# Performance work log

Measured on AMD Instinct MI355X. Metric: run time of the kernel, lower is better.

The kernel has to match this reference:

```python
import jax, jax.numpy as jnp
import numpy as np

N = 200000
C = 128
VOX = 0.05
EPS = 1e-5
OFFSETS = np.array([[dz, dy, dx] for dz in (-1, 0, 1) for dy in (-1, 0, 1) for dx in (-1, 0, 1)], dtype=np.int64)


def setup_inputs() -> dict:
    key = jax.random.key(0)
    ks = jax.random.split(key, 8)
    gp = jax.random.normal(ks[0], (N, 14), jnp.float32)
    # ---- voxelization tables (int constants, computed once in numpy) ----
    pts = np.asarray(gp[:, :3], dtype=np.float64)
    vc = np.floor(pts / VOX).astype(np.int64)
    vc = vc - vc.min(axis=0)
    mx = vc.max(axis=0) + 1
    h = vc[:, 0] * mx[1] * mx[2] + vc[:, 1] * mx[2] + vc[:, 2]
    uh, inv = np.unique(h, return_inverse=True)
    M = int(uh.shape[0])
    vcoord = np.zeros((M, 3), np.int64)
    vcoord[inv] = vc  # coords identical for same hash
    nbr_idx = np.zeros((M, 27), np.int32)
    nbr_mask = np.zeros((M, 27), np.float32)
    for o in range(27):
        nc = vcoord + OFFSETS[o]
        inb = (nc >= 0).all(1) & (nc < mx).all(1)
        nh = nc[:, 0] * mx[1] * mx[2] + nc[:, 1] * mx[2] + nc[:, 2]
        pos = np.clip(np.searchsorted(uh, nh), 0, M - 1)
        found = inb & (uh[pos] == nh)
        nbr_idx[:, o] = np.where(found, pos, 0)
        nbr_mask[:, o] = found.astype(np.float32)
    s = 0.05
    return {
        'gaussian_params': gp,
        'w_enc': jax.random.normal(ks[1], (14, C), jnp.float32) * s,
        'b_enc': jnp.zeros((C,), jnp.float32),
        'ln_g': jnp.ones((C,), jnp.float32),
        'ln_b': jnp.zeros((C,), jnp.float32),
        'conv_w': jax.random.normal(ks[2], (4, 27, C, C), jnp.float32) * s,
        'bn_g': jnp.ones((4, C), jnp.float32),
        'bn_b': jnp.zeros((4, C), jnp.float32),
        'w1': jax.random.normal(ks[3], (C, C // 2), jnp.float32) * s,
        'b1': jnp.zeros((C // 2,), jnp.float32),
        'w2': jax.random.normal(ks[4], (C // 2, 14), jnp.float32) * s,
        'b2': jnp.zeros((14,), jnp.float32),
        'nbr_mask': jnp.asarray(nbr_mask),
        'inv_idx': jnp.asarray(inv.astype(np.int32)),
        'nbr_idx': jnp.asarray(nbr_idx),
        'num_voxels': M,
    }


def _bn(x, g, b):
    m = x.mean(0)
    v = x.var(0)
    return (x - m) * jax.lax.rsqrt(v + EPS) * g + b


def _subm(x, W, nbr_idx, nbr_mask):
    # submanifold 3x3x3 conv: sum over 27 offsets of masked neighbor gather @ W[o]
    out = jnp.zeros_like(x)
    for o in range(27):
        out = out + (x[nbr_idx[:, o]] * nbr_mask[:, o:o + 1]) @ W[o]
    return out


def _forward(gp, w_enc, b_enc, ln_g, ln_b, conv_w, bn_g, bn_b, w1, b1, w2, b2, nbr_mask, inv_idx, nbr_idx, num_voxels):
    # input encoder: Linear -> LayerNorm -> ReLU
    f = gp @ w_enc + b_enc
    mu = f.mean(-1, keepdims=True)
    var = f.var(-1, keepdims=True)
    f = jax.nn.relu((f - mu) * jax.lax.rsqrt(var + EPS) * ln_g + ln_b)
    # points -> voxels: segment mean (the op the torch code did with a Python loop)
    cnt = jax.ops.segment_sum(jnp.ones((gp.shape[0],), f.dtype), inv_idx, num_segments=num_voxels)
    x = jax.ops.segment_sum(f, inv_idx, num_segments=num_voxels) / cnt[:, None]
    # 2 residual sparse conv blocks (BN uses batch stats, training-mode forward)
    for blk in range(2):
        idn = x
        out = _subm(x, conv_w[2 * blk], nbr_idx, nbr_mask)
        out = jax.nn.relu(_bn(out, bn_g[2 * blk], bn_b[2 * blk]))
        out = _subm(out, conv_w[2 * blk + 1], nbr_idx, nbr_mask)
        x = jax.nn.relu(_bn(out, bn_g[2 * blk + 1], bn_b[2 * blk + 1]) + idn)
    # voxels -> points, output head, residual add
    pf = x[inv_idx]
    delta = jax.nn.relu(pf @ w1 + b1) @ w2 + b2
    return gp[:, :14] + delta


def reference(gaussian_params, w_enc, b_enc, ln_g, ln_b, conv_w, bn_g, bn_b, w1, b1, w2, b2, nbr_mask, inv_idx, nbr_idx, num_voxels):
    return _forward(gaussian_params, w_enc, b_enc, ln_g, ln_b, conv_w, bn_g, bn_b, w1, b1, w2, b2, nbr_mask, inv_idx, nbr_idx, num_voxels)
```

## Files before the change

kernel.cpp:

```cpp
#include <hip/hip_runtime.h>

typedef __bf16 bf16x8 __attribute__((ext_vector_type(8)));
typedef float f32x16 __attribute__((ext_vector_type(16)));

#define LN_EPS 1e-5f
#define AS1 __attribute__((address_space(1)))
#define AS3 __attribute__((address_space(3)))

__device__ __forceinline__ unsigned f2bf_rne(float f) {
    unsigned x = __float_as_uint(f);
    return (x + 0x7fffu + ((x >> 16) & 1u)) >> 16;
}

__device__ __forceinline__ float bf2f(unsigned short u) {
    return __uint_as_float((unsigned)u << 16);
}

__global__ void pack_w_kernel(const float* __restrict__ cw, unsigned short* __restrict__ Wp, int E) {
    int idx = blockIdx.x * 256 + threadIdx.x;
    if (idx >= E) return;
    float v = cw[idx];
    int n  = idx & 127;
    int c  = (idx >> 7) & 127;
    int oc = idx >> 14;
    Wp[oc * 16384 + (c >> 3) * 1024 + n * 8 + (c & 7)] = (unsigned short)f2bf_rne(v);
}

__global__ void pack_w1_kernel(const float* __restrict__ w1, unsigned short* __restrict__ Wp1) {
    int idx = blockIdx.x * 256 + threadIdx.x;
    if (idx >= 8192) return;
    int k = idx >> 6, n = idx & 63;
    Wp1[(k >> 3) * 512 + n * 8 + (k & 7)] = (unsigned short)f2bf_rne(w1[k * 64 + n]);
}

__global__ void prep_nbr_kernel(const int* __restrict__ nbr_idx, const float* __restrict__ nbr_mask,
                                int* __restrict__ T, unsigned* __restrict__ act, int M) {
    int m = blockIdx.x * 256 + threadIdx.x;
    if (m >= M) return;
    unsigned bits = 0;
#pragma unroll
    for (int o = 0; o < 27; ++o) {
        bool f = nbr_mask[m * 27 + o] != 0.f;
        int g = f ? nbr_idx[m * 27 + o] : M;
        T[o * M + m] = g;
        bits |= (f ? 1u : 0u) << o;
    }
    atomicOr(&act[m >> 7], bits);
}

__global__ __launch_bounds__(256) void encode_kernel(
    const float* __restrict__ gp, const float* __restrict__ w_enc,
    const float* __restrict__ b_enc, const float* __restrict__ ln_g,
    const float* __restrict__ ln_b, const int* __restrict__ inv_idx,
    float* __restrict__ vsum, float* __restrict__ cnt, int N)
{
    int p = blockIdx.x * 4 + (threadIdx.x >> 6);
    int lane = threadIdx.x & 63;
    if (p >= N) return;
    float gv[14];
#pragma unroll
    for (int i = 0; i < 14; ++i) gv[i] = gp[p * 14 + i];
    float f0 = b_enc[lane], f1 = b_enc[lane + 64];
#pragma unroll
    for (int i = 0; i < 14; ++i) {
        f0 = fmaf(gv[i], w_enc[i * 128 + lane], f0);
        f1 = fmaf(gv[i], w_enc[i * 128 + lane + 64], f1);
    }
    float s = f0 + f1;
#pragma unroll
    for (int off = 32; off; off >>= 1) s += __shfl_xor(s, off);
    float mean = s * 0.0078125f;
    float d0 = f0 - mean, d1 = f1 - mean;
    float v = d0 * d0 + d1 * d1;
#pragma unroll
    for (int off = 32; off; off >>= 1) v += __shfl_xor(v, off);
    float rs = rsqrtf(v * 0.0078125f + LN_EPS);
    float h0 = d0 * rs * ln_g[lane] + ln_b[lane];
    float h1 = d1 * rs * ln_g[lane + 64] + ln_b[lane + 64];
    h0 = h0 > 0.f ? h0 : 0.f;
    h1 = h1 > 0.f ? h1 : 0.f;
    int vx = inv_idx[p];
    atomicAdd(&vsum[vx * 128 + lane], h0);
    atomicAdd(&vsum[vx * 128 + lane + 64], h1);
    if (lane == 0) atomicAdd(&cnt[vx], 1.0f);
}

__global__ void vox_mean_kernel(const float* __restrict__ vsum, const float* __restrict__ cnt,
                                unsigned short* __restrict__ out, int total4) {
    int idx = blockIdx.x * 256 + threadIdx.x;
    if (idx >= total4) return;
    int e0 = idx * 4;
    float r = 1.f / cnt[e0 >> 7];
    float4 v = *(const float4*)(vsum + e0);
    uint2 pk;
    pk.x = f2bf_rne(v.x * r) | (f2bf_rne(v.y * r) << 16);
    pk.y = f2bf_rne(v.z * r) | (f2bf_rne(v.w * r) << 16);
    *(uint2*)(out + e0) = pk;
}

__global__ __launch_bounds__(256, 4) void subm_conv_kernel(
    const unsigned short* __restrict__ xin,
    const unsigned short* __restrict__ Wp,
    const int* __restrict__ T, const unsigned* __restrict__ act,
    float* __restrict__ yout, float* __restrict__ stats, int M)
{
    __shared__ uint4 Ws[2048];

    const int tid = threadIdx.x;
    const int lane = tid & 63;
    const int w = tid >> 6;
    const int m0 = blockIdx.x * 128;
    const int rw = w * 32;
    const int q = lane >> 5;
    const int l31 = lane & 31;
    int myrow = m0 + rw + l31;
    if (myrow >= M) myrow = M - 1;

    f32x16 acc[4];
#pragma unroll
    for (int t = 0; t < 4; ++t)
#pragma unroll
        for (int r = 0; r < 16; ++r) acc[t][r] = 0.f;

    const uint4* xin4 = (const uint4*)xin;
    unsigned amask = act[blockIdx.x];

    while (amask) {
        int o = __ffs(amask) - 1;
        amask &= amask - 1;

        __syncthreads();

        const uint4* WpO4 = (const uint4*)Wp + o * 2048;
#pragma unroll
        for (int rep = 0; rep < 8; ++rep) {
            __builtin_amdgcn_global_load_lds(
                (const AS1 unsigned int*)(WpO4 + rep * 256 + tid),
                (AS3 unsigned int*)(Ws + rep * 256 + w * 64), 16, 0, 0);
        }

        int g = T[o * M + myrow];
        uint4 af[8];
#pragma unroll
        for (int j = 0; j < 8; ++j) af[j] = xin4[g * 16 + 2 * j + q];

        __syncthreads();

#pragma unroll
        for (int ks = 0; ks < 8; ++ks) {
            int kb = (ks << 1) | q;
            bf16x8 a = *(const bf16x8*)&af[ks];
#pragma unroll
            for (int tn = 0; tn < 4; ++tn) {
                bf16x8 b = ((const bf16x8*)Ws)[kb * 128 + tn * 32 + l31];
                acc[tn] = __builtin_amdgcn_mfma_f32_32x32x16_bf16(a, b, acc[tn], 0, 0, 0);
            }
        }
    }

#pragma unroll
    for (int tn = 0; tn < 4; ++tn) {
        int col = tn * 32 + l31;
        float s = 0.f, sq = 0.f;
#pragma unroll
        for (int r = 0; r < 16; ++r) {
            int rloc = (r & 3) + 8 * (r >> 2) + 4 * q + rw;
            int grow = m0 + rloc;
            float v = acc[tn][r];
            if (grow < M) yout[grow * 128 + col] = v;
            s += v; sq += v * v;
        }
        s += __shfl_xor(s, 32);
        sq += __shfl_xor(sq, 32);
        if (lane < 32) {
            atomicAdd(&stats[col], s);
            atomicAdd(&stats[128 + col], sq);
        }
    }
}

__global__ void bn_relu_kernel(const float* __restrict__ y, const float* __restrict__ stats,
                               const float* __restrict__ g, const float* __restrict__ b,
                               unsigned short* __restrict__ out, int total4, float invM) {
    int idx = blockIdx.x * 256 + threadIdx.x;
    if (idx >= total4) return;
    int e0 = idx * 4;
    int c0 = e0 & 127;
    float4 yv = *(const float4*)(y + e0);
    float h[4];
    const float* yp = (const float*)&yv;
#pragma unroll
    for (int j = 0; j < 4; ++j) {
        int c = c0 + j;
        float mean = stats[c] * invM;
        float var = stats[128 + c] * invM - mean * mean;
        float sc = g[c] * rsqrtf(var + LN_EPS);
        float sh = b[c] - mean * sc;
        float vv = yp[j] * sc + sh;
        h[j] = vv > 0.f ? vv : 0.f;
    }
    uint2 pk;
    pk.x = f2bf_rne(h[0]) | (f2bf_rne(h[1]) << 16);
    pk.y = f2bf_rne(h[2]) | (f2bf_rne(h[3]) << 16);
    *(uint2*)(out + e0) = pk;
}

__global__ void bn_relu_res_kernel(const float* __restrict__ y, const float* __restrict__ stats,
                                   const float* __restrict__ g, const float* __restrict__ b,
                                   const unsigned short* __restrict__ idn,
                                   unsigned short* __restrict__ out, int total4, float invM) {
    int idx = blockIdx.x * 256 + threadIdx.x;
    if (idx >= total4) return;
    int e0 = idx * 4;
    int c0 = e0 & 127;
    float4 yv = *(const float4*)(y + e0);
    uint2 iv = *(const uint2*)(idn + e0);
    float id[4];
    id[0] = __uint_as_float(iv.x << 16);
    id[1] = __uint_as_float(iv.x & 0xffff0000u);
    id[2] = __uint_as_float(iv.y << 16);
    id[3] = __uint_as_float(iv.y & 0xffff0000u);
    float h[4];
    const float* yp = (const float*)&yv;
#pragma unroll
    for (int j = 0; j < 4; ++j) {
        int c = c0 + j;
        float mean = stats[c] * invM;
        float var = stats[128 + c] * invM - mean * mean;
        float sc = g[c] * rsqrtf(var + LN_EPS);
        float sh = b[c] - mean * sc;
        float vv = yp[j] * sc + sh + id[j];
        h[j] = vv > 0.f ? vv : 0.f;
    }
    uint2 pk;
    pk.x = f2bf_rne(h[0]) | (f2bf_rne(h[1]) << 16);
    pk.y = f2bf_rne(h[2]) | (f2bf_rne(h[3]) << 16);
    *(uint2*)(out + e0) = pk;
}

__global__ __launch_bounds__(256) void head_vox_kernel(
    const unsigned short* __restrict__ A,
    const unsigned short* __restrict__ Wp1,
    const float* __restrict__ b1, const float* __restrict__ w2,
    const float* __restrict__ b2, float* __restrict__ Dv, int M)
{
    __shared__ uint4 W1s[1024];
    __shared__ unsigned short Hs[8192];
    __shared__ float w2s[896];

    const int tid = threadIdx.x;
    const int lane = tid & 63;
    const int w = tid >> 6;
    const int m0 = blockIdx.x * 128;
    const int rw = w * 32;
    const int q = lane >> 5;
    const int l31 = lane & 31;
    int myrow = m0 + rw + l31;
    if (myrow > M) myrow = M;

#pragma unroll
    for (int rep = 0; rep < 4; ++rep) {
        __builtin_amdgcn_global_load_lds(
            (const AS1 unsigned int*)((const uint4*)Wp1 + rep * 256 + tid),
            (AS3 unsigned int*)(W1s + rep * 256 + w * 64), 16, 0, 0);
    }
    for (int i = tid; i < 896; i += 256) w2s[i] = w2[i];

    const uint4* xin4 = (const uint4*)A;
    uint4 af[8];
#pragma unroll
    for (int j = 0; j < 8; ++j) af[j] = xin4[myrow * 16 + 2 * j + q];

    f32x16 acc[2];
#pragma unroll
    for (int t = 0; t < 2; ++t)
#pragma unroll
        for (int r = 0; r < 16; ++r) acc[t][r] = 0.f;

    __syncthreads();

#pragma unroll
    for (int ks = 0; ks < 8; ++ks) {
        int kb = (ks << 1) | q;
        bf16x8 a = *(const bf16x8*)&af[ks];
#pragma unroll
        for (int tn = 0; tn < 2; ++tn) {
            bf16x8 b = ((const bf16x8*)W1s)[kb * 64 + tn * 32 + l31];
            acc[tn] = __builtin_amdgcn_mfma_f32_32x32x16_bf16(a, b, acc[tn], 0, 0, 0);
        }
    }

#pragma unroll
    for (int tn = 0; tn < 2; ++tn) {
        int col = tn * 32 + l31;
        float bias = b1[col];
        int ch = col >> 3, ce = col & 7;
#pragma unroll
        for (int r = 0; r < 16; ++r) {
            int rloc = (r & 3) + 8 * (r >> 2) + 4 * q + rw;
            float v = acc[tn][r] + bias;
            v = v > 0.f ? v : 0.f;
            Hs[rloc * 64 + (ch ^ (rloc & 7)) * 8 + ce] = (unsigned short)f2bf_rne(v);
        }
    }
    __syncthreads();

    int r2 = tid >> 1;
    int c0 = (tid & 1) * 7;
    float o[7];
#pragma unroll
    for (int j = 0; j < 7; ++j) o[j] = b2[c0 + j];
#pragma unroll
    for (int c = 0; c < 8; ++c) {
        bf16x8 hv = ((const bf16x8*)Hs)[r2 * 8 + (c ^ (r2 & 7))];
#pragma unroll
        for (int e = 0; e < 8; ++e) {
            float h = bf2f(((const unsigned short*)&hv)[e]);
            int k = c * 8 + e;
#pragma unroll
            for (int j = 0; j < 7; ++j) o[j] = fmaf(h, w2s[k * 14 + c0 + j], o[j]);
        }
    }
    int grow = m0 + r2;
    if (grow < M) {
#pragma unroll
        for (int j = 0; j < 7; ++j) Dv[grow * 14 + c0 + j] = o[j];
    }
}

__global__ void head_scatter_kernel(const float* __restrict__ gp, const float* __restrict__ Dv,
                                    const int* __restrict__ inv_idx, float* __restrict__ out, int N) {
    int p = blockIdx.x * 256 + threadIdx.x;
    if (p >= N) return;
    int vx = inv_idx[p];
#pragma unroll
    for (int c = 0; c < 14; ++c) out[p * 14 + c] = gp[p * 14 + c] + Dv[vx * 14 + c];
}

extern "C" void kernel_launch(void* const* d_in, const int* in_sizes, int n_in,
                              void* d_out, int out_size, void* d_ws, size_t ws_size,
                              hipStream_t stream) {
    const float* gp       = (const float*)d_in[0];
    const float* w_enc    = (const float*)d_in[1];
    const float* b_enc    = (const float*)d_in[2];
    const float* ln_g     = (const float*)d_in[3];
    const float* ln_b     = (const float*)d_in[4];
    const float* conv_w   = (const float*)d_in[5];
    const float* bn_g     = (const float*)d_in[6];
    const float* bn_b     = (const float*)d_in[7];
    const float* w1       = (const float*)d_in[8];
    const float* b1       = (const float*)d_in[9];
    const float* w2       = (const float*)d_in[10];
    const float* b2       = (const float*)d_in[11];
    const float* nbr_mask = (const float*)d_in[12];
    const int*   inv_idx  = (const int*)d_in[13];
    const int*   nbr_idx  = (const int*)d_in[14];

    const int N = in_sizes[0] / 14;
    const int M = in_sizes[12] / 27;
    const int ntiles = (M + 127) / 128;

    char* ws = (char*)d_ws;
    size_t off = 0;
    unsigned short* Wp = (unsigned short*)(ws + off); off += (size_t)4 * 27 * 16384 * 2;
    unsigned short* A  = (unsigned short*)(ws + off); off += (size_t)(M + 1) * 128 * 2;
    unsigned short* H  = (unsigned short*)(ws + off); off += (size_t)(M + 1) * 128 * 2;
    float* Yraw  = (float*)(ws + off);
    size_t zoff = off;
    off += (size_t)M * 128 * 4;
    float* cnt   = (float*)(ws + off); off += (size_t)M * 4;
    float* stats = (float*)(ws + off); off += 4 * 256 * 4;
    unsigned* act = (unsigned*)(ws + off); off += (size_t)ntiles * 4;
    size_t zbytes = off - zoff;
    int* T = (int*)(ws + off); off += (size_t)27 * M * 4;
    unsigned short* Wp1 = (unsigned short*)(ws + off); off += 8192 * 2;
    float* Dv = Yraw;

    hipMemsetAsync(Yraw, 0, zbytes, stream);
    hipMemsetAsync(A + (size_t)M * 128, 0, 256, stream);
    hipMemsetAsync(H + (size_t)M * 128, 0, 256, stream);

    const int E = 4 * 27 * 128 * 128;
    pack_w_kernel<<<(E + 255) / 256, 256, 0, stream>>>(conv_w, Wp, E);
    pack_w1_kernel<<<32, 256, 0, stream>>>(w1, Wp1);
    prep_nbr_kernel<<<(M + 255) / 256, 256, 0, stream>>>(nbr_idx, nbr_mask, T, act, M);
    encode_kernel<<<(N + 3) / 4, 256, 0, stream>>>(gp, w_enc, b_enc, ln_g, ln_b, inv_idx, Yraw, cnt, N);
    const int total4 = M * 32;
    vox_mean_kernel<<<(total4 + 255) / 256, 256, 0, stream>>>(Yraw, cnt, A, total4);

    const float invM = 1.f / (float)M;
    for (int blk = 0; blk < 2; ++blk) {
        int c0 = 2 * blk, c1 = 2 * blk + 1;
        subm_conv_kernel<<<ntiles, 256, 0, stream>>>(
            A, Wp + (size_t)c0 * 27 * 16384, T, act, Yraw, stats + c0 * 256, M);
        bn_relu_kernel<<<(total4 + 255) / 256, 256, 0, stream>>>(
            Yraw, stats + c0 * 256, bn_g + c0 * 128, bn_b + c0 * 128, H, total4, invM);
        subm_conv_kernel<<<ntiles, 256, 0, stream>>>(
            H, Wp + (size_t)c1 * 27 * 16384, T, act, Yraw, stats + c1 * 256, M);
        bn_relu_res_kernel<<<(total4 + 255) / 256, 256, 0, stream>>>(
            Yraw, stats + c1 * 256, bn_g + c1 * 128, bn_b + c1 * 128, A, A, total4, invM);
    }
    head_vox_kernel<<<ntiles, 256, 0, stream>>>(A, Wp1, b1, w2, b2, Dv, M);
    head_scatter_kernel<<<(N + 255) / 256, 256, 0, stream>>>(gp, Dv, inv_idx, (float*)d_out, N);
}
```

Measured before the change: 1.518 ms.

## Double-buffer conv weight tiles in LDS and prefetch next offset's gathers

The sparse conv kernel now keeps two LDS weight buffers. While the MFMA loop runs on the current one, it issues the async global-to-LDS copy of the next active offset's weights and register-prefetches that offset's gathered input rows and neighbour index. This halves the barriers per offset and hides load latency behind compute. The cost is double the LDS, about 32 extra VGPRs, and a launch bound relaxed from 4 to 2 blocks per CU, so occupancy drops. It also zeroes out-of-range rows before they enter the BN statistics, because clamped rows were previously counted in them.

```diff
diff --git a/kernel.cpp b/kernel.cpp
--- a/kernel.cpp
+++ b/kernel.cpp
@@ -98,13 +98,13 @@
     *(uint2*)(out + e0) = pk;
 }
 
-__global__ __launch_bounds__(256, 4) void subm_conv_kernel(
+__global__ __launch_bounds__(256, 2) void subm_conv_kernel(
     const unsigned short* __restrict__ xin,
     const unsigned short* __restrict__ Wp,
     const int* __restrict__ T, const unsigned* __restrict__ act,
     float* __restrict__ yout, float* __restrict__ stats, int M)
 {
-    __shared__ uint4 Ws[2048];
+    __shared__ uint4 Ws[4096];
 
     const int tid = threadIdx.x;
     const int lane = tid & 63;
@@ -125,36 +125,71 @@
     const uint4* xin4 = (const uint4*)xin;
     unsigned amask = act[blockIdx.x];
 
-    while (amask) {
+    if (amask) {
         int o = __ffs(amask) - 1;
         amask &= amask - 1;
-
-        __syncthreads();
-
-        const uint4* WpO4 = (const uint4*)Wp + o * 2048;
-#pragma unroll
-        for (int rep = 0; rep < 8; ++rep) {
-            __builtin_amdgcn_global_load_lds(
-                (const AS1 unsigned int*)(WpO4 + rep * 256 + tid),
-                (AS3 unsigned int*)(Ws + rep * 256 + w * 64), 16, 0, 0);
-        }
-
-        int g = T[o * M + myrow];
+        {
+            const uint4* WpO4 = (const uint4*)Wp + o * 2048;
+#pragma unroll
+            for (int rep = 0; rep < 8; ++rep) {
+                __builtin_amdgcn_global_load_lds(
+                    (const AS1 unsigned int*)(WpO4 + rep * 256 + tid),
+                    (AS3 unsigned int*)(Ws + rep * 256 + w * 64), 16, 0, 0);
+            }
+        }
+        int g0 = T[o * M + myrow];
         uint4 af[8];
 #pragma unroll
-        for (int j = 0; j < 8; ++j) af[j] = xin4[g * 16 + 2 * j + q];
-
-        __syncthreads();
-
-#pragma unroll
-        for (int ks = 0; ks < 8; ++ks) {
-            int kb = (ks << 1) | q;
-            bf16x8 a = *(const bf16x8*)&af[ks];
-#pragma unroll
-            for (int tn = 0; tn < 4; ++tn) {
-                bf16x8 b = ((const bf16x8*)Ws)[kb * 128 + tn * 32 + l31];
-                acc[tn] = __builtin_amdgcn_mfma_f32_32x32x16_bf16(a, b, acc[tn], 0, 0, 0);
+        for (int j = 0; j < 8; ++j) af[j] = xin4[g0 * 16 + 2 * j + q];
+
+        int onext = -1, gnext = 0;
+        if (amask) {
+            onext = __ffs(amask) - 1;
+            amask &= amask - 1;
+            gnext = T[onext * M + myrow];
+        }
+
+        int buf = 0;
+        while (true) {
+            __syncthreads();
+
+            uint4 af2[8];
+            int onn = -1, gnext2 = 0;
+            if (onext >= 0) {
+                const uint4* WpN4 = (const uint4*)Wp + onext * 2048;
+#pragma unroll
+                for (int rep = 0; rep < 8; ++rep) {
+                    __builtin_amdgcn_global_load_lds(
+                        (const AS1 unsigned int*)(WpN4 + rep * 256 + tid),
+                        (AS3 unsigned int*)(Ws + (buf ^ 1) * 2048 + rep * 256 + w * 64), 16, 0, 0);
+                }
+#pragma unroll
+                for (int j = 0; j < 8; ++j) af2[j] = xin4[gnext * 16 + 2 * j + q];
+                if (amask) {
+                    onn = __ffs(amask) - 1;
+                    amask &= amask - 1;
+                    gnext2 = T[onn * M + myrow];
+                }
             }
+
+            const bf16x8* WsB = (const bf16x8*)(Ws + buf * 2048);
+#pragma unroll
+            for (int ks = 0; ks < 8; ++ks) {
+                int kb = (ks << 1) | q;
+                bf16x8 a = *(const bf16x8*)&af[ks];
+#pragma unroll
+                for (int tn = 0; tn < 4; ++tn) {
+                    bf16x8 b = WsB[kb * 128 + tn * 32 + l31];
+                    acc[tn] = __builtin_amdgcn_mfma_f32_32x32x16_bf16(a, b, acc[tn], 0, 0, 0);
+                }
+            }
+
+            if (onext < 0) break;
+#pragma unroll
+            for (int j = 0; j < 8; ++j) af[j] = af2[j];
+            gnext = gnext2;
+            onext = onn;
+            buf ^= 1;
         }
     }
 
@@ -166,7 +201,7 @@
         for (int r = 0; r < 16; ++r) {
             int rloc = (r & 3) + 8 * (r >> 2) + 4 * q + rw;
             int grow = m0 + rloc;
-            float v = acc[tn][r];
+            float v = (grow < M) ? acc[tn][r] : 0.f;
             if (grow < M) yout[grow * 128 + col] = v;
             s += v; sq += v * v;
         }
```

Result: no change. 1.500 ms (-1.1%).

## Double-buffer weight staging and neighbor gathers in sparse conv MFMA loop

Applied to the files above, without the earlier changes.

The submanifold conv loop is software-pipelined. The next offset's weights load into a second LDS buffer, and its neighbor rows load into a second register set, while MFMAs run on the current offset. A manual vmcnt wait plus barrier replaces the two syncthreads. Tiles are remapped so each XCD gets a contiguous range, and out-of-range rows are zeroed before the BN statistics. The cost is double the LDS, more registers, and launch bounds lowered from 4 to 2 blocks per CU, which reduces occupancy.

```diff
diff --git a/kernel.cpp b/kernel.cpp
--- a/kernel.cpp
+++ b/kernel.cpp
@@ -98,18 +98,63 @@
     *(uint2*)(out + e0) = pk;
 }
 
-__global__ __launch_bounds__(256, 4) void subm_conv_kernel(
+#define STAGE_W(OFF, BUFSEL)                                                          \
+    {                                                                                 \
+        const uint4* WpO4 = (const uint4*)Wp + (OFF) * 2048;                          \
+        _Pragma("unroll")                                                             \
+        for (int rep = 0; rep < 8; ++rep) {                                           \
+            __builtin_amdgcn_global_load_lds(                                         \
+                (const AS1 unsigned int*)(WpO4 + rep * 256 + tid),                    \
+                (AS3 unsigned int*)(Ws + (BUFSEL) * 2048 + rep * 256 + w * 64),       \
+                16, 0, 0);                                                            \
+        }                                                                             \
+    }                                                                                 \
+    __builtin_amdgcn_sched_barrier(0);
+
+#define GATHER_A(AF, G)                                                               \
+    _Pragma("unroll")                                                                 \
+    for (int j = 0; j < 8; ++j) (AF)[j] = xin4[(G) * 16 + 2 * j + q];
+
+#define MFMA_PHASE(AF, BUFSEL)                                                        \
+    {                                                                                 \
+        const bf16x8* WsB = (const bf16x8*)(Ws + (BUFSEL) * 2048);                    \
+        _Pragma("unroll")                                                             \
+        for (int ks = 0; ks < 8; ++ks) {                                              \
+            int kb = (ks << 1) | q;                                                   \
+            bf16x8 a = *(const bf16x8*)&(AF)[ks];                                     \
+            _Pragma("unroll")                                                         \
+            for (int tn = 0; tn < 4; ++tn) {                                          \
+                bf16x8 b = WsB[kb * 128 + tn * 32 + l31];                             \
+                acc[tn] = __builtin_amdgcn_mfma_f32_32x32x16_bf16(a, b, acc[tn], 0, 0, 0); \
+            }                                                                         \
+        }                                                                             \
+    }
+
+#define SYNC_POINT()                                                                  \
+    __builtin_amdgcn_sched_barrier(0);                                                \
+    asm volatile("s_waitcnt vmcnt(8)" ::: "memory");                                  \
+    __builtin_amdgcn_s_barrier();                                                     \
+    __builtin_amdgcn_sched_barrier(0);
+
+__global__ __launch_bounds__(256, 2) void subm_conv_kernel(
     const unsigned short* __restrict__ xin,
     const unsigned short* __restrict__ Wp,
     const int* __restrict__ T, const unsigned* __restrict__ act,
     float* __restrict__ yout, float* __restrict__ stats, int M)
 {
-    __shared__ uint4 Ws[2048];
+    __shared__ uint4 Ws[4096];
 
     const int tid = threadIdx.x;
     const int lane = tid & 63;
     const int w = tid >> 6;
-    const int m0 = blockIdx.x * 128;
+
+    const int nwg = gridDim.x;
+    const int orig = blockIdx.x;
+    const int xcd = orig & 7;
+    const int q8 = nwg >> 3, r8 = nwg & 7;
+    const int tile = (xcd < r8 ? xcd * (q8 + 1) : r8 * (q8 + 1) + (xcd - r8) * q8) + (orig >> 3);
+
+    const int m0 = tile * 128;
     const int rw = w * 32;
     const int q = lane >> 5;
     const int l31 = lane & 31;
@@ -123,38 +168,39 @@
         for (int r = 0; r < 16; ++r) acc[t][r] = 0.f;
 
     const uint4* xin4 = (const uint4*)xin;
-    unsigned amask = act[blockIdx.x];
-
-    while (amask) {
-        int o = __ffs(amask) - 1;
-        amask &= amask - 1;
-
-        __syncthreads();
-
-        const uint4* WpO4 = (const uint4*)Wp + o * 2048;
-#pragma unroll
-        for (int rep = 0; rep < 8; ++rep) {
-            __builtin_amdgcn_global_load_lds(
-                (const AS1 unsigned int*)(WpO4 + rep * 256 + tid),
-                (AS3 unsigned int*)(Ws + rep * 256 + w * 64), 16, 0, 0);
-        }
-
-        int g = T[o * M + myrow];
-        uint4 af[8];
-#pragma unroll
-        for (int j = 0; j < 8; ++j) af[j] = xin4[g * 16 + 2 * j + q];
-
-        __syncthreads();
-
-#pragma unroll
-        for (int ks = 0; ks < 8; ++ks) {
-            int kb = (ks << 1) | q;
-            bf16x8 a = *(const bf16x8*)&af[ks];
-#pragma unroll
-            for (int tn = 0; tn < 4; ++tn) {
-                bf16x8 b = ((const bf16x8*)Ws)[kb * 128 + tn * 32 + l31];
-                acc[tn] = __builtin_amdgcn_mfma_f32_32x32x16_bf16(a, b, acc[tn], 0, 0, 0);
+    unsigned amask = act[tile];
+
+    if (amask) {
+        uint4 afA[8], afB[8];
+
+        int oA = __ffs(amask) - 1; amask &= amask - 1;
+        STAGE_W(oA, 0);
+        int gA = T[oA * M + myrow];
+        GATHER_A(afA, gA);
+        int oB = -1, gB = 0;
+        if (amask) { oB = __ffs(amask) - 1; amask &= amask - 1; gB = T[oB * M + myrow]; }
+
+        while (true) {
+            SYNC_POINT();
+            int oC = -1, gC = 0;
+            if (oB >= 0) {
+                STAGE_W(oB, 1);
+                GATHER_A(afB, gB);
+                if (amask) { oC = __ffs(amask) - 1; amask &= amask - 1; gC = T[oC * M + myrow]; }
             }
+            MFMA_PHASE(afA, 0);
+            if (oB < 0) break;
+
+            SYNC_POINT();
+            int oD = -1, gD = 0;
+            if (oC >= 0) {
+                STAGE_W(oC, 0);
+                GATHER_A(afA, gC);
+                if (amask) { oD = __ffs(amask) - 1; amask &= amask - 1; gD = T[oD * M + myrow]; }
+            }
+            MFMA_PHASE(afB, 1);
+            if (oC < 0) break;
+            oB = oD; gB = gD;
         }
     }
 
@@ -166,7 +212,7 @@
         for (int r = 0; r < 16; ++r) {
             int rloc = (r & 3) + 8 * (r >> 2) + 4 * q + rw;
             int grow = m0 + rloc;
-            float v = acc[tn][r];
+            float v = (grow < M) ? acc[tn][r] : 0.f;
             if (grow < M) yout[grow * 128 + col] = v;
             s += v; sq += v * v;
         }
```

New measurement: 1.533 ms. Within noise of the previous version (+1.0%).

## Double-buffer conv weights, 256-row tiles with two accumulator sets, XCD-aware tile remap

Applied to the files above, without the earlier changes.

The sparse conv kernel now handles 256 voxel rows per workgroup, with each wave computing two 32-row MFMA tiles that share the same LDS weight fragments. Weights for the next active offset are prefetched into a second LDS buffer while the current one is consumed, and the next neighbor indices are loaded early, so only one barrier is needed per offset. Block indices are remapped so that contiguous tiles land on the same XCD, and MFMA sections run at raised wave priority. In exchange the kernel uses twice the LDS and accumulator registers, and occupancy drops to two workgroups per CU. The active-offset mask is coarsened to 256-row tiles, so more inactive offsets may be computed.

```diff
diff --git a/kernel.cpp b/kernel.cpp
--- a/kernel.cpp
+++ b/kernel.cpp
@@ -45,7 +45,7 @@
         T[o * M + m] = g;
         bits |= (f ? 1u : 0u) << o;
     }
-    atomicOr(&act[m >> 7], bits);
+    atomicOr(&act[m >> 8], bits);
 }
 
 __global__ __launch_bounds__(256) void encode_kernel(
@@ -98,63 +98,98 @@
     *(uint2*)(out + e0) = pk;
 }
 
-__global__ __launch_bounds__(256, 4) void subm_conv_kernel(
+#define STAGE_W(OFF, BUFSEL)                                                          \
+    {                                                                                 \
+        const uint4* WpO4 = (const uint4*)Wp + (OFF) * 2048;                          \
+        _Pragma("unroll")                                                             \
+        for (int rep = 0; rep < 8; ++rep) {                                           \
+            __builtin_amdgcn_global_load_lds(                                         \
+                (const AS1 unsigned int*)(WpO4 + rep * 256 + tid),                    \
+                (AS3 unsigned int*)(Ws + (BUFSEL) * 2048 + rep * 256 + w * 64),       \
+                16, 0, 0);                                                            \
+        }                                                                             \
+    }
+
+#define GATHER_A(AF, G)                                                               \
+    _Pragma("unroll")                                                                 \
+    for (int j = 0; j < 8; ++j) (AF)[j] = xin4[(G) * 16 + 2 * j + q];
+
+__global__ __launch_bounds__(256, 2) void subm_conv_kernel(
     const unsigned short* __restrict__ xin,
     const unsigned short* __restrict__ Wp,
     const int* __restrict__ T, const unsigned* __restrict__ act,
     float* __restrict__ yout, float* __restrict__ stats, int M)
 {
-    __shared__ uint4 Ws[2048];
+    __shared__ uint4 Ws[4096];
 
     const int tid = threadIdx.x;
     const int lane = tid & 63;
     const int w = tid >> 6;
-    const int m0 = blockIdx.x * 128;
-    const int rw = w * 32;
+
+    const int nwg = gridDim.x;
+    const int orig = blockIdx.x;
+    const int xcd = orig & 7;
+    const int q8 = nwg >> 3, r8 = nwg & 7;
+    const int tile = (xcd < r8 ? xcd * (q8 + 1) : r8 * (q8 + 1) + (xcd - r8) * q8) + (orig >> 3);
+
+    const int m0 = tile * 256;
+    const int rw = w * 64;
     const int q = lane >> 5;
     const int l31 = lane & 31;
-    int myrow = m0 + rw + l31;
-    if (myrow >= M) myrow = M - 1;
-
-    f32x16 acc[4];
+    int row0 = m0 + rw + l31;
+    int row1 = row0 + 32;
+    if (row0 >= M) row0 = M - 1;
+    if (row1 >= M) row1 = M - 1;
+
+    f32x16 acc0[4], acc1[4];
 #pragma unroll
     for (int t = 0; t < 4; ++t)
 #pragma unroll
-        for (int r = 0; r < 16; ++r) acc[t][r] = 0.f;
+        for (int r = 0; r < 16; ++r) { acc0[t][r] = 0.f; acc1[t][r] = 0.f; }
 
     const uint4* xin4 = (const uint4*)xin;
-    unsigned amask = act[blockIdx.x];
-
-    while (amask) {
-        int o = __ffs(amask) - 1;
-        amask &= amask - 1;
-
-        __syncthreads();
-
-        const uint4* WpO4 = (const uint4*)Wp + o * 2048;
-#pragma unroll
-        for (int rep = 0; rep < 8; ++rep) {
-            __builtin_amdgcn_global_load_lds(
-                (const AS1 unsigned int*)(WpO4 + rep * 256 + tid),
-                (AS3 unsigned int*)(Ws + rep * 256 + w * 64), 16, 0, 0);
-        }
-
-        int g = T[o * M + myrow];
-        uint4 af[8];
-#pragma unroll
-        for (int j = 0; j < 8; ++j) af[j] = xin4[g * 16 + 2 * j + q];
-
-        __syncthreads();
-
-#pragma unroll
-        for (int ks = 0; ks < 8; ++ks) {
-            int kb = (ks << 1) | q;
-            bf16x8 a = *(const bf16x8*)&af[ks];
-#pragma unroll
-            for (int tn = 0; tn < 4; ++tn) {
-                bf16x8 b = ((const bf16x8*)Ws)[kb * 128 + tn * 32 + l31];
-                acc[tn] = __builtin_amdgcn_mfma_f32_32x32x16_bf16(a, b, acc[tn], 0, 0, 0);
+    unsigned amask = act[tile];
+
+    if (amask) {
+        int o = __ffs(amask) - 1; amask &= amask - 1;
+        STAGE_W(o, 0);
+        int g0 = T[o * M + row0];
+        int g1 = T[o * M + row1];
+        int buf = 0;
+
+        while (true) {
+            int onext = -1;
+            if (amask) { onext = __ffs(amask) - 1; amask &= amask - 1; }
+
+            __syncthreads();
+
+            if (onext >= 0) STAGE_W(onext, buf ^ 1);
+
+            uint4 af0[8], af1[8];
+            GATHER_A(af0, g0);
+            GATHER_A(af1, g1);
+
+            int gn0 = 0, gn1 = 0;
+            if (onext >= 0) { gn0 = T[onext * M + row0]; gn1 = T[onext * M + row1]; }
+
+            const bf16x8* WsB = (const bf16x8*)(Ws + buf * 2048);
+            __builtin_amdgcn_s_setprio(1);
+#pragma unroll
+            for (int ks = 0; ks < 8; ++ks) {
+                int kb = (ks << 1) | q;
+                bf16x8 a0 = *(const bf16x8*)&af0[ks];
+                bf16x8 a1 = *(const bf16x8*)&af1[ks];
+#pragma unroll
+                for (int tn = 0; tn < 4; ++tn) {
+                    bf16x8 b = WsB[kb * 128 + tn * 32 + l31];
+                    acc0[tn] = __builtin_amdgcn_mfma_f32_32x32x16_bf16(a0, b, acc0[tn], 0, 0, 0);
+                    acc1[tn] = __builtin_amdgcn_mfma_f32_32x32x16_bf16(a1, b, acc1[tn], 0, 0, 0);
+                }
             }
+            __builtin_amdgcn_s_setprio(0);
+
+            if (onext < 0) break;
+            o = onext; g0 = gn0; g1 = gn1; buf ^= 1;
         }
     }
 
@@ -166,7 +201,15 @@
         for (int r = 0; r < 16; ++r) {
             int rloc = (r & 3) + 8 * (r >> 2) + 4 * q + rw;
             int grow = m0 + rloc;
-            float v = acc[tn][r];
+            float v = (grow < M) ? acc0[tn][r] : 0.f;
+            if (grow < M) yout[grow * 128 + col] = v;
+            s += v; sq += v * v;
+        }
+#pragma unroll
+        for (int r = 0; r < 16; ++r) {
+            int rloc = (r & 3) + 8 * (r >> 2) + 4 * q + rw + 32;
+            int grow = m0 + rloc;
+            float v = (grow < M) ? acc1[tn][r] : 0.f;
             if (grow < M) yout[grow * 128 + col] = v;
             s += v; sq += v * v;
         }
@@ -359,6 +402,7 @@
     const int N = in_sizes[0] / 14;
     const int M = in_sizes[12] / 27;
     const int ntiles = (M + 127) / 128;
+    const int ntiles256 = (M + 255) / 256;
 
     char* ws = (char*)d_ws;
     size_t off = 0;
@@ -391,11 +435,11 @@
     const float invM = 1.f / (float)M;
     for (int blk = 0; blk < 2; ++blk) {
         int c0 = 2 * blk, c1 = 2 * blk + 1;
-        subm_conv_kernel<<<ntiles, 256, 0, stream>>>(
+        subm_conv_kernel<<<ntiles256, 256, 0, stream>>>(
             A, Wp + (size_t)c0 * 27 * 16384, T, act, Yraw, stats + c0 * 256, M);
         bn_relu_kernel<<<(total4 + 255) / 256, 256, 0, stream>>>(
             Yraw, stats + c0 * 256, bn_g + c0 * 128, bn_b + c0 * 128, H, total4, invM);
-        subm_conv_kernel<<<ntiles, 256, 0, stream>>>(
+        subm_conv_kernel<<<ntiles256, 256, 0, stream>>>(
             H, Wp + (size_t)c1 * 27 * 16384, T, act, Yraw, stats + c1 * 256, M);
         bn_relu_res_kernel<<<(total4 + 255) / 256, 256, 0, stream>>>(
             Yraw, stats + c1 * 256, bn_g + c1 * 128, bn_b + c1 * 128, A, A, total4, invM);
```

Result: faster. 1.480 ms (-2.5%).
